# Optimization experiments

Measured on AMD Instinct MI355X. Metric: run time of the kernel, lower is better.

The kernel has to match this reference:

```python
import jax, jax.numpy as jnp
import numpy as np

DIM = 256
B = 8
H = 56
W = 56
K = 2
EPS = 1e-5  # torch BatchNorm2d default eps


def _conv1x1(x, w, b):
    # x: [B,C,H,W], w: [O,C], b: [O]
    return jnp.einsum('oc,bchw->bohw', w, x) + b[None, :, None, None]


def _bn(x, g, be, m, v):
    # inference-mode BatchNorm2d with running stats
    s = g / jnp.sqrt(v + EPS)
    return x * s[None, :, None, None] + (be - m * s)[None, :, None, None]


def _grapher(x, w1, b1, g1, be1, m1, v1, wg, bg, gg, beg, mg, vg, w2, b2, g2, be2, m2, v2):
    # fc1: 1x1 conv + BN
    h = _bn(_conv1x1(x, w1, b1), g1, be1, m1, v1)
    Hh, Ww = h.shape[2], h.shape[3]
    # MRConv4d: running max over circular-shift differences
    # torch.cat([x[:,:,-i:,:], x[:,:,:-i,:]], dim=2) == jnp.roll(x, i, axis=2)
    xj = jnp.zeros_like(h)

    def body_h(c, i):
        return jnp.maximum(c, h - jnp.roll(h, i, axis=2)), None

    xj, _ = jax.lax.scan(body_h, xj, jnp.arange(K, Hh, K))

    def body_w(c, i):
        return jnp.maximum(c, h - jnp.roll(h, i, axis=3)), None

    xj, _ = jax.lax.scan(body_w, xj, jnp.arange(K, Ww, K))

    cat = jnp.concatenate([h, xj], axis=1)  # [B, 2*dim, H, W]
    # MRConv4d.nn: Conv2d(2*dim, 2*dim, 1) -> BN(2*dim) -> GELU (exact erf)
    g = jax.nn.gelu(_bn(_conv1x1(cat, wg, bg), gg, beg, mg, vg), approximate=False)
    # fc2: Conv2d(2*dim, dim, 1) + BN(dim), then residual
    return _bn(_conv1x1(g, w2, b2), g2, be2, m2, v2) + x


def setup_inputs() -> dict:
    key = jax.random.key(0)
    ks = jax.random.split(key, 12)
    d, d2 = DIM, 2 * DIM

    def w(k, o, c):
        return jax.random.normal(k, (o, c), jnp.float32) * np.float32(1.0 / np.sqrt(c))

    return {
        'x': jax.random.normal(ks[0], (B, d, H, W), jnp.float32),
        'w1': w(ks[1], d, d), 'b1': jnp.zeros((d,), jnp.float32),
        'g1': jnp.ones((d,), jnp.float32), 'be1': jnp.zeros((d,), jnp.float32),
        'm1': jax.random.normal(ks[2], (d,), jnp.float32) * 0.1,
        'v1': jax.random.uniform(ks[3], (d,), jnp.float32, 0.5, 1.5),
        'wg': w(ks[4], d2, d2), 'bg': jnp.zeros((d2,), jnp.float32),
        'gg': jnp.ones((d2,), jnp.float32), 'beg': jnp.zeros((d2,), jnp.float32),
        'mg': jax.random.normal(ks[5], (d2,), jnp.float32) * 0.1,
        'vg': jax.random.uniform(ks[6], (d2,), jnp.float32, 0.5, 1.5),
        'w2': w(ks[7], d, d2), 'b2': jnp.zeros((d,), jnp.float32),
        'g2': jnp.ones((d,), jnp.float32), 'be2': jnp.zeros((d,), jnp.float32),
        'm2': jax.random.normal(ks[8], (d,), jnp.float32) * 0.1,
        'v2': jax.random.uniform(ks[9], (d,), jnp.float32, 0.5, 1.5),
    }


def reference(x, w1, b1, g1, be1, m1, v1, wg, bg, gg, beg, mg, vg, w2, b2, g2, be2, m2, v2):
    return _grapher(x, w1, b1, g1, be1, m1, v1, wg, bg, gg, beg, mg, vg, w2, b2, g2, be2, m2, v2)
```

## Files before the change

### kernel.cpp

```cpp
#include <hip/hip_runtime.h>
#include <math.h>

#define SPB 3136
#define NB 8
#define MTOT (NB*SPB)
#define EPS 1e-5f

typedef unsigned short u16;
typedef __attribute__((ext_vector_type(8))) short short8;
typedef __attribute__((ext_vector_type(4))) float float4v;

__device__ __forceinline__ float b2f(u16 v){ unsigned u=((unsigned)v)<<16; float f; __builtin_memcpy(&f,&u,4); return f; }
__device__ __forceinline__ u16 f2b(float f){ unsigned u; __builtin_memcpy(&u,&f,4); u += 0x7fffu + ((u>>16)&1u); return (u16)(u>>16); }
__device__ __forceinline__ float gelu_f(float z){ return 0.5f*z*(1.0f+erff(z*0.70710678118654752f)); }

__device__ __forceinline__ void gll16(const u16* g, u16* l){
  __builtin_amdgcn_global_load_lds((const __attribute__((address_space(1))) void*)g,
                                   (__attribute__((address_space(3))) void*)l, 16, 0, 0);
}

__global__ void prep_consts_k(const float* b1,const float* g1,const float* be1,const float* m1,const float* v1,
                              const float* bg,const float* gg,const float* beg,const float* mg,const float* vg,
                              const float* b2,const float* g2,const float* be2,const float* m2,const float* v2,
                              float* cst){
  int i = threadIdx.x;
  if (i < 256) {
    float s = g1[i]*rsqrtf(v1[i]+EPS);
    cst[i] = s; cst[256+i] = b1[i]*s + be1[i] - m1[i]*s;
    float s2 = g2[i]*rsqrtf(v2[i]+EPS);
    cst[1536+i] = s2; cst[1792+i] = b2[i]*s2 + be2[i] - m2[i]*s2;
  }
  float s = gg[i]*rsqrtf(vg[i]+EPS);
  cst[512+i] = s; cst[1024+i] = bg[i]*s + beg[i] - mg[i]*s;
}

__global__ void conv_w_k(const float* __restrict__ w1,const float* __restrict__ wg,const float* __restrict__ w2,
                         u16* __restrict__ w1b,u16* __restrict__ wgb,u16* __restrict__ w2b){
  int i = blockIdx.x*256 + threadIdx.x;
  if (i < 65536)  w1b[i] = f2b(w1[i]);
  if (i < 262144) wgb[i] = f2b(wg[i]);
  if (i < 131072) w2b[i] = f2b(w2[i]);
}

__global__ void transpose_x_k(const float* __restrict__ x, u16* __restrict__ xt){
  __shared__ float t[32][33];
  int b = blockIdx.z, ct = blockIdx.y, st = blockIdx.x;
  int ts = threadIdx.x, tc = threadIdx.y;
  #pragma unroll
  for (int i=0;i<4;i++){
    int c = tc + i*8;
    t[c][ts] = x[((size_t)(b*256 + ct*32 + c))*SPB + st*32 + ts];
  }
  __syncthreads();
  #pragma unroll
  for (int i=0;i<4;i++){
    int r = tc + i*8;
    xt[((size_t)(b*SPB + st*32 + r))*256 + ct*32 + ts] = f2b(t[ts][r]);
  }
}

__global__ void rowmin_k(const u16* __restrict__ cat, float* __restrict__ rmin){
  int b = blockIdx.x/56, y = blockIdx.x%56, c = threadIdx.x;
  float mE=3.4e38f, mO=3.4e38f;
  const u16* base = cat + ((size_t)(b*SPB + y*56))*512 + c;
  for (int x=0;x<56;x+=2){
    mE = fminf(mE, b2f(base[(size_t)x*512]));
    mO = fminf(mO, b2f(base[(size_t)(x+1)*512]));
  }
  rmin[((size_t)(b*2+0)*56 + y)*256 + c]=mE;
  rmin[((size_t)(b*2+1)*56 + y)*256 + c]=mO;
}
__global__ void colmin_k(const u16* __restrict__ cat, float* __restrict__ cmin){
  int b = blockIdx.x/56, x = blockIdx.x%56, c = threadIdx.x;
  float mE=3.4e38f, mO=3.4e38f;
  const u16* base = cat + ((size_t)(b*SPB + x))*512 + c;
  for (int y=0;y<56;y+=2){
    mE = fminf(mE, b2f(base[(size_t)(y*56)*512]));
    mO = fminf(mO, b2f(base[(size_t)((y+1)*56)*512]));
  }
  cmin[((size_t)(b*2+0)*56 + x)*256 + c]=mE;
  cmin[((size_t)(b*2+1)*56 + x)*256 + c]=mO;
}
__global__ void xj_k(u16* __restrict__ cat, const float* __restrict__ rmin, const float* __restrict__ cmin){
  int b = blockIdx.y, s = blockIdx.x, c = threadIdx.x;
  int y = s/56, x = s%56;
  size_t idx = ((size_t)(b*SPB + s))*512;
  float h = b2f(cat[idx + c]);
  float m = fminf(cmin[((size_t)(b*2+(y&1))*56 + x)*256 + c],
                  rmin[((size_t)(b*2+(x&1))*56 + y)*256 + c]);
  cat[idx + 256 + c] = f2b(fmaxf(0.0f, h - m));
}

template<int KTOT, int EPI>
__global__ __launch_bounds__(256) void gemm_k(
    const u16* __restrict__ Ain, const u16* __restrict__ Wt,
    const float* __restrict__ scale, const float* __restrict__ bias,
    void* __restrict__ outp, const float* __restrict__ resid)
{
  __shared__ __align__(16) u16 smem[16896];
  u16* As = smem;
  u16* Bs = smem + 4096;
  const int tid = threadIdx.x;
  const int m0 = blockIdx.x * 128;
  const int o0 = blockIdx.y * 128;
  const int lane = tid & 63, wid = tid >> 6;
  const int quad = lane >> 4, l16 = lane & 15;
  const int wm = wid & 1, wn = wid >> 1;

  float4v acc[4][4];
  #pragma unroll
  for (int i=0;i<4;i++)
    #pragma unroll
    for (int j=0;j<4;j++) acc[i][j] = (float4v){0.f,0.f,0.f,0.f};

  const int row = tid >> 2, q8 = (tid & 3) * 8;
  const u16* ga0 = Ain + ((size_t)(m0 + row))*KTOT + q8;
  const u16* ga1 = ga0 + (size_t)64*KTOT;
  const u16* gb0 = Wt  + ((size_t)(o0 + row))*KTOT + q8;
  const u16* gb1 = gb0 + (size_t)64*KTOT;
  u16* la0 = As + tid*8;
  u16* la1 = As + 2048 + tid*8;
  u16* lb0 = Bs + tid*8;
  u16* lb1 = Bs + 2048 + tid*8;

  for (int kt = 0; kt < KTOT; kt += 32) {
    gll16(ga0 + kt, la0);
    gll16(ga1 + kt, la1);
    gll16(gb0 + kt, lb0);
    gll16(gb1 + kt, lb1);
    __syncthreads();
    short8 af[4], bfr[4];
    #pragma unroll
    for (int im=0;im<4;im++) af[im]  = *(const short8*)&As[(wm*64+im*16+l16)*32 + quad*8];
    #pragma unroll
    for (int in=0;in<4;in++) bfr[in] = *(const short8*)&Bs[(wn*64+in*16+l16)*32 + quad*8];
    #pragma unroll
    for (int im=0;im<4;im++)
      #pragma unroll
      for (int in=0;in<4;in++)
        acc[im][in] = __builtin_amdgcn_mfma_f32_16x16x32_bf16(af[im], bfr[in], acc[im][in], 0, 0, 0);
    __syncthreads();
  }

  if (EPI == 1 || EPI == 2) {
    u16* tile = smem;
    #pragma unroll
    for (int im=0;im<4;im++)
      #pragma unroll
      for (int in=0;in<4;in++){
        int ol = wn*64 + in*16 + l16;
        float sc = scale[o0+ol], bi = bias[o0+ol];
        #pragma unroll
        for (int r=0;r<4;r++){
          float v = acc[im][in][r]*sc + bi;
          if (EPI==2) v = gelu_f(v);
          tile[(wm*64+im*16+quad*4+r)*128 + ol] = f2b(v);
        }
      }
    __syncthreads();
    u16* op = (u16*)outp;
    #pragma unroll
    for (int p=0;p<8;p++){
      int chunk = p*256 + tid;
      int rr = chunk >> 4, off = (chunk & 15)*8;
      *(uint4*)&op[((size_t)(m0 + rr))*512 + o0 + off] = *(const uint4*)&tile[rr*128 + off];
    }
  } else {
    float* ftile = (float*)smem;
    float* op = (float*)outp;
    #pragma unroll
    for (int h=0; h<2; h++){
      if (wn == h){
        #pragma unroll
        for (int im=0;im<4;im++)
          #pragma unroll
          for (int in=0;in<4;in++){
            int c64 = in*16 + l16;
            int og = o0 + h*64 + c64;
            float sc = scale[og], bi = bias[og];
            float4v v;
            #pragma unroll
            for (int r=0;r<4;r++) v[r] = acc[im][in][r]*sc + bi;
            *(float4v*)&ftile[c64*132 + wm*64 + im*16 + quad*4] = v;
          }
      }
      __syncthreads();
      #pragma unroll
      for (int p=0;p<8;p++){
        int chunk = p*256 + tid;
        int rr = chunk >> 5, off = (chunk & 31)*4;
        int m = m0 + off;
        int b = m / SPB, s = m - b*SPB;
        size_t g = ((size_t)(b*256 + o0 + h*64 + rr))*SPB + s;
        float4v v = *(const float4v*)&ftile[rr*132 + off];
        v.x += resid[g]; v.y += resid[g+1]; v.z += resid[g+2]; v.w += resid[g+3];
        *(float4v*)&op[g] = v;
      }
      __syncthreads();
    }
  }
}

extern "C" void kernel_launch(void* const* d_in, const int* in_sizes, int n_in,
                              void* d_out, int out_size, void* d_ws, size_t ws_size,
                              hipStream_t stream)
{
  const float* x  = (const float*)d_in[0];
  const float* w1 = (const float*)d_in[1];
  const float* b1 = (const float*)d_in[2];
  const float* g1 = (const float*)d_in[3];
  const float* be1= (const float*)d_in[4];
  const float* m1 = (const float*)d_in[5];
  const float* v1 = (const float*)d_in[6];
  const float* wg = (const float*)d_in[7];
  const float* bg = (const float*)d_in[8];
  const float* gg = (const float*)d_in[9];
  const float* beg= (const float*)d_in[10];
  const float* mg = (const float*)d_in[11];
  const float* vg = (const float*)d_in[12];
  const float* w2 = (const float*)d_in[13];
  const float* b2 = (const float*)d_in[14];
  const float* g2 = (const float*)d_in[15];
  const float* be2= (const float*)d_in[16];
  const float* m2 = (const float*)d_in[17];
  const float* v2 = (const float*)d_in[18];

  char* ws = (char*)d_ws;
  size_t off = 0;
  auto alloc = [&](size_t bytes){ void* p = ws + off; off += (bytes + 255) & ~(size_t)255; return p; };
  u16* xt    = (u16*)alloc((size_t)MTOT*256*2);
  u16* catt  = (u16*)alloc((size_t)MTOT*512*2);
  u16* gt    = (u16*)alloc((size_t)MTOT*512*2);
  u16* w1b   = (u16*)alloc((size_t)65536*2);
  u16* wgb   = (u16*)alloc((size_t)262144*2);
  u16* w2b   = (u16*)alloc((size_t)131072*2);
  float* cst = (float*)alloc((size_t)2048*4);
  float* rmin= (float*)alloc((size_t)NB*2*56*256*4);
  float* cmin= (float*)alloc((size_t)NB*2*56*256*4);

  hipLaunchKernelGGL(prep_consts_k, dim3(1), dim3(512), 0, stream,
                     b1,g1,be1,m1,v1, bg,gg,beg,mg,vg, b2,g2,be2,m2,v2, cst);
  hipLaunchKernelGGL(conv_w_k, dim3(1024), dim3(256), 0, stream, w1,wg,w2, w1b,wgb,w2b);
  hipLaunchKernelGGL(transpose_x_k, dim3(98,8,8), dim3(32,8), 0, stream, x, xt);
  hipLaunchKernelGGL((gemm_k<256,1>), dim3(196,2), dim3(256), 0, stream,
                     xt, w1b, cst+0, cst+256, (void*)catt, (const float*)nullptr);
  hipLaunchKernelGGL(rowmin_k, dim3(NB*56), dim3(256), 0, stream, catt, rmin);
  hipLaunchKernelGGL(colmin_k, dim3(NB*56), dim3(256), 0, stream, catt, cmin);
  hipLaunchKernelGGL(xj_k, dim3(SPB, NB), dim3(256), 0, stream, catt, rmin, cmin);
  hipLaunchKernelGGL((gemm_k<512,2>), dim3(196,4), dim3(256), 0, stream,
                     catt, wgb, cst+512, cst+1024, (void*)gt, (const float*)nullptr);
  hipLaunchKernelGGL((gemm_k<512,3>), dim3(196,2), dim3(256), 0, stream,
                     gt, w2b, cst+1536, cst+1792, d_out, x);
}
```

Before: 205.9 us.

## Load GEMM operands directly from global into registers, dropping LDS staging

```diff
diff --git a/kernel.cpp b/kernel.cpp
--- a/kernel.cpp
+++ b/kernel.cpp
@@ -13,11 +13,6 @@
 __device__ __forceinline__ float b2f(u16 v){ unsigned u=((unsigned)v)<<16; float f; __builtin_memcpy(&f,&u,4); return f; }
 __device__ __forceinline__ u16 f2b(float f){ unsigned u; __builtin_memcpy(&u,&f,4); u += 0x7fffu + ((u>>16)&1u); return (u16)(u>>16); }
 __device__ __forceinline__ float gelu_f(float z){ return 0.5f*z*(1.0f+erff(z*0.70710678118654752f)); }
-
-__device__ __forceinline__ void gll16(const u16* g, u16* l){
-  __builtin_amdgcn_global_load_lds((const __attribute__((address_space(1))) void*)g,
-                                   (__attribute__((address_space(3))) void*)l, 16, 0, 0);
-}
 
 __global__ void prep_consts_k(const float* b1,const float* g1,const float* be1,const float* m1,const float* v1,
                               const float* bg,const float* gg,const float* beg,const float* mg,const float* vg,
@@ -98,63 +93,50 @@
     void* __restrict__ outp, const float* __restrict__ resid)
 {
   __shared__ __align__(16) u16 smem[16896];
-  u16* As = smem;
-  u16* Bs = smem + 4096;
   const int tid = threadIdx.x;
   const int m0 = blockIdx.x * 128;
   const int o0 = blockIdx.y * 128;
   const int lane = tid & 63, wid = tid >> 6;
   const int quad = lane >> 4, l16 = lane & 15;
-  const int wm = wid & 1, wn = wid >> 1;
-
-  float4v acc[4][4];
-  #pragma unroll
-  for (int i=0;i<4;i++)
-    #pragma unroll
-    for (int j=0;j<4;j++) acc[i][j] = (float4v){0.f,0.f,0.f,0.f};
-
-  const int row = tid >> 2, q8 = (tid & 3) * 8;
-  const u16* ga0 = Ain + ((size_t)(m0 + row))*KTOT + q8;
-  const u16* ga1 = ga0 + (size_t)64*KTOT;
-  const u16* gb0 = Wt  + ((size_t)(o0 + row))*KTOT + q8;
-  const u16* gb1 = gb0 + (size_t)64*KTOT;
-  u16* la0 = As + tid*8;
-  u16* la1 = As + 2048 + tid*8;
-  u16* lb0 = Bs + tid*8;
-  u16* lb1 = Bs + 2048 + tid*8;
-
+
+  float4v acc[2][8];
+  #pragma unroll
+  for (int i=0;i<2;i++)
+    #pragma unroll
+    for (int j=0;j<8;j++) acc[i][j] = (float4v){0.f,0.f,0.f,0.f};
+
+  const u16* aBase = Ain + ((size_t)(m0 + wid*32 + l16))*KTOT + quad*8;
+  const u16* bBase = Wt  + ((size_t)(o0 + l16))*KTOT + quad*8;
+
+  #pragma unroll
   for (int kt = 0; kt < KTOT; kt += 32) {
-    gll16(ga0 + kt, la0);
-    gll16(ga1 + kt, la1);
-    gll16(gb0 + kt, lb0);
-    gll16(gb1 + kt, lb1);
-    __syncthreads();
-    short8 af[4], bfr[4];
-    #pragma unroll
-    for (int im=0;im<4;im++) af[im]  = *(const short8*)&As[(wm*64+im*16+l16)*32 + quad*8];
-    #pragma unroll
-    for (int in=0;in<4;in++) bfr[in] = *(const short8*)&Bs[(wn*64+in*16+l16)*32 + quad*8];
-    #pragma unroll
-    for (int im=0;im<4;im++)
-      #pragma unroll
-      for (int in=0;in<4;in++)
-        acc[im][in] = __builtin_amdgcn_mfma_f32_16x16x32_bf16(af[im], bfr[in], acc[im][in], 0, 0, 0);
-    __syncthreads();
+    short8 af[2], bf[8];
+    #pragma unroll
+    for (int im=0;im<2;im++)
+      af[im] = *(const short8*)(aBase + (size_t)im*16*KTOT + kt);
+    #pragma unroll
+    for (int in=0;in<8;in++)
+      bf[in] = *(const short8*)(bBase + (size_t)in*16*KTOT + kt);
+    #pragma unroll
+    for (int im=0;im<2;im++)
+      #pragma unroll
+      for (int in=0;in<8;in++)
+        acc[im][in] = __builtin_amdgcn_mfma_f32_16x16x32_bf16(af[im], bf[in], acc[im][in], 0, 0, 0);
   }
 
   if (EPI == 1 || EPI == 2) {
     u16* tile = smem;
     #pragma unroll
-    for (int im=0;im<4;im++)
-      #pragma unroll
-      for (int in=0;in<4;in++){
-        int ol = wn*64 + in*16 + l16;
+    for (int im=0;im<2;im++)
+      #pragma unroll
+      for (int in=0;in<8;in++){
+        int ol = in*16 + l16;
         float sc = scale[o0+ol], bi = bias[o0+ol];
         #pragma unroll
         for (int r=0;r<4;r++){
           float v = acc[im][in][r]*sc + bi;
           if (EPI==2) v = gelu_f(v);
-          tile[(wm*64+im*16+quad*4+r)*128 + ol] = f2b(v);
+          tile[(wid*32+im*16+quad*4+r)*128 + ol] = f2b(v);
         }
       }
     __syncthreads();
@@ -170,20 +152,18 @@
     float* op = (float*)outp;
     #pragma unroll
     for (int h=0; h<2; h++){
-      if (wn == h){
+      #pragma unroll
+      for (int im=0;im<2;im++)
         #pragma unroll
-        for (int im=0;im<4;im++)
+        for (int in=4*h; in<4*h+4; in++){
+          int c64 = in*16 + l16 - h*64;
+          int og = o0 + h*64 + c64;
+          float sc = scale[og], bi = bias[og];
+          float4v v;
           #pragma unroll
-          for (int in=0;in<4;in++){
-            int c64 = in*16 + l16;
-            int og = o0 + h*64 + c64;
-            float sc = scale[og], bi = bias[og];
-            float4v v;
-            #pragma unroll
-            for (int r=0;r<4;r++) v[r] = acc[im][in][r]*sc + bi;
-            *(float4v*)&ftile[c64*132 + wm*64 + im*16 + quad*4] = v;
-          }
-      }
+          for (int r=0;r<4;r++) v[r] = acc[im][in][r]*sc + bi;
+          *(float4v*)&ftile[c64*132 + wid*32 + im*16 + quad*4] = v;
+        }
       __syncthreads();
       #pragma unroll
       for (int p=0;p<8;p++){
```

Result: slower. 283.8 us (+37.8%).
